# Optimization experiments

Hardware: AMD Instinct MI355X
Metric: run time of the kernel (lower is better)

Reference implementation:

```python
import jax, jax.numpy as jnp
import numpy as np

B, N, D, H = 32, 8192, 128, 128


def setup_inputs() -> dict:
    key = jax.random.key(0)
    ks = jax.random.split(key, 9)
    s = lambda k, shp, fan: jax.random.normal(k, shp, jnp.float32) / np.sqrt(fan)
    return {
        "x": jax.random.normal(ks[0], (B, N, D), jnp.float32),
        "Wg1": s(ks[1], (D, H), D), "bg1": jnp.zeros((H,), jnp.float32),
        "Wg2": s(ks[2], (H, 1), H), "bg2": jnp.zeros((1,), jnp.float32),
        "Wn1": s(ks[3], (D, H), D), "bn1": jnp.zeros((H,), jnp.float32),
        "Wn2": s(ks[4], (H, H), H), "bn2": jnp.zeros((H,), jnp.float32),
    }


def reference(x, Wg1, bg1, Wg2, bg2, Wn1, bn1, Wn2, bn2):
    # gate_nn: Linear -> SiLU -> Linear(->1); scores per node
    gate = jnp.einsum("bnd,dh->bnh", x, Wg1) + bg1
    gate = jax.nn.silu(gate)
    gate = jnp.einsum("bnh,ho->bno", gate, Wg2) + bg2  # [B,N,1]
    # nn: Linear -> SiLU -> Linear; transformed node features
    h = jax.nn.silu(jnp.einsum("bnd,dh->bnh", x, Wn1) + bn1)
    h = jnp.einsum("bnh,hk->bnk", h, Wn2) + bn2  # [B,N,H]
    # segment softmax over nodes of each graph (segments == batch dim here)
    attn = jax.nn.softmax(gate, axis=1)  # [B,N,1]
    # weighted-sum pooling per graph
    return jnp.sum(attn * h, axis=1)  # [B,H]
```

## Files before the change

kernel.cpp:

```cpp
#include <hip/hip_runtime.h>

#define B_ 32
#define N_ 8192
#define D_ 128
#define H_ 128
#define R_ (B_ * N_)

#define NBLK 4096

typedef _Float16 f16;
typedef __attribute__((ext_vector_type(4))) _Float16 f16x4;
typedef __attribute__((ext_vector_type(8))) _Float16 f16x8;
typedef __attribute__((ext_vector_type(4))) float f32x4;

static constexpr size_t WPACK_OFF = 0;
static constexpr size_t VPART_OFF = 65536;
static constexpr size_t SPART_OFF = VPART_OFF + (size_t)NBLK * 128 * 4;

__device__ __forceinline__ float silu_f(float v) {
    return v * __builtin_amdgcn_rcpf(1.0f + __expf(-v));
}

__device__ __forceinline__ f32x4 mfma16(f16x8 a, f16x8 b, f32x4 c) {
    return __builtin_amdgcn_mfma_f32_16x16x32_f16(a, b, c, 0, 0, 0);
}

__global__ void k0_prepack(const float* __restrict__ Wg1,
                           const float* __restrict__ Wn1,
                           f16* __restrict__ wp) {
    int tid = blockIdx.x * 256 + threadIdx.x;
    int m    = tid >> 14;
    int r    = tid & 16383;
    int j    = r & 7;
    int lane = (r >> 3) & 63;
    int kc   = (r >> 9) & 3;
    int nt   = r >> 11;
    int k = kc * 32 + (lane >> 4) * 8 + j;
    int n = nt * 16 + (lane & 15);
    const float* W = m ? Wn1 : Wg1;
    wp[tid] = (f16)W[k * 128 + n];
}

__global__ __launch_bounds__(256, 3) void k1_fused(
        const float* __restrict__ x,
        const float* __restrict__ bg1, const float* __restrict__ wg2,
        const float* __restrict__ bg2, const float* __restrict__ bn1,
        const f16* __restrict__ wp,
        float* __restrict__ vpart, float* __restrict__ spart) {
    __shared__ f16 xlds[64 * 128];
    __shared__ float gpart[4][64];

    const int tid  = threadIdx.x;
    const int w    = tid >> 6;
    const int lane = tid & 63;
    const int q    = lane >> 4;
    const int c    = lane & 15;

    const long rowbase = (long)blockIdx.x * 64;
    const float4* xg = (const float4*)x + rowbase * 32;
    float4 xv[8];
#pragma unroll
    for (int s = 0; s < 8; ++s) xv[s] = xg[s * 256 + tid];

    const f16x8* wpv = (const f16x8*)wp;
    f16x8 fg1[2][4], fn1[2][4];
#pragma unroll
    for (int s = 0; s < 2; ++s)
#pragma unroll
        for (int kc = 0; kc < 4; ++kc) {
            int base = ((2 * w + s) * 4 + kc) * 64 + lane;
            fg1[s][kc] = wpv[base];
            fn1[s][kc] = wpv[2048 + base];
        }
    float bg1q[2][4], wg2q[2][4], bn1q[2][4];
#pragma unroll
    for (int s = 0; s < 2; ++s)
#pragma unroll
        for (int r = 0; r < 4; ++r) {
            int col = (2 * w + s) * 16 + q * 4 + r;
            bg1q[s][r] = bg1[col];
            wg2q[s][r] = wg2[col];
            bn1q[s][r] = bn1[col];
        }
    const float bg2v = bg2[0];

    const int loh_e = (q * 16 + (c ^ q)) * 8;
    const int loh_o = (q * 16 + (c ^ (q | 4))) * 8;

#pragma unroll
    for (int s = 0; s < 8; ++s) {
        int e   = s * 256 + tid;
        int row = e >> 5, c4 = e & 31;
        int mt = row >> 4, cc = row & 15;
        int kc = c4 >> 3, qq = (c4 >> 1) & 3, j = (c4 & 1) * 4;
        int sw = (c4 >> 1) & 7;
        float4 vv = xv[s];
        f16x4 hv = {(f16)vv.x, (f16)vv.y, (f16)vv.z, (f16)vv.w};
        *(f16x4*)&xlds[((mt * 4 + kc) * 64 + qq * 16 + (cc ^ sw)) * 8 + j] = hv;
    }
    __syncthreads();

    f16x4 hq[4][2];
#pragma unroll
    for (int mt = 0; mt < 4; ++mt) {
        f16x8 a[4];
#pragma unroll
        for (int kc = 0; kc < 4; ++kc)
            a[kc] = *(const f16x8*)&xlds[(mt * 4 + kc) * 512 +
                                         ((kc & 1) ? loh_o : loh_e)];
        f32x4 ag[2] = {{0.f,0.f,0.f,0.f},{0.f,0.f,0.f,0.f}};
        f32x4 an[2] = {{0.f,0.f,0.f,0.f},{0.f,0.f,0.f,0.f}};
#pragma unroll
        for (int kc = 0; kc < 4; ++kc) {
#pragma unroll
            for (int s = 0; s < 2; ++s) {
                ag[s] = mfma16(fg1[s][kc], a[kc], ag[s]);
                an[s] = mfma16(fn1[s][kc], a[kc], an[s]);
            }
        }
#pragma unroll
        for (int s = 0; s < 2; ++s) {
            f16x4 h4;
#pragma unroll
            for (int r = 0; r < 4; ++r) h4[r] = (f16)silu_f(an[s][r] + bn1q[s][r]);
            hq[mt][s] = h4;
        }
        float p = 0.f;
#pragma unroll
        for (int s = 0; s < 2; ++s)
#pragma unroll
            for (int r = 0; r < 4; ++r)
                p += silu_f(ag[s][r] + bg1q[s][r]) * wg2q[s][r];
        p += __shfl_xor(p, 16);
        p += __shfl_xor(p, 32);
        if (lane < 16) gpart[w][mt * 16 + lane] = p;
    }
    __syncthreads();

    float e4[4];
#pragma unroll
    for (int mt = 0; mt < 4; ++mt) {
        float g = bg2v + gpart[0][mt * 16 + c] + gpart[1][mt * 16 + c]
                       + gpart[2][mt * 16 + c] + gpart[3][mt * 16 + c];
        e4[mt] = __expf(g);
    }

    float V[2][4] = {{0.f,0.f,0.f,0.f},{0.f,0.f,0.f,0.f}};
#pragma unroll
    for (int mt = 0; mt < 4; ++mt)
#pragma unroll
        for (int s = 0; s < 2; ++s)
#pragma unroll
            for (int r = 0; r < 4; ++r)
                V[s][r] += e4[mt] * (float)hq[mt][s][r];

#pragma unroll
    for (int m = 1; m < 16; m <<= 1)
#pragma unroll
        for (int s = 0; s < 2; ++s)
#pragma unroll
            for (int r = 0; r < 4; ++r) V[s][r] += __shfl_xor(V[s][r], m);
    if (c == 0) {
#pragma unroll
        for (int s = 0; s < 2; ++s) {
            float4 o = {V[s][0], V[s][1], V[s][2], V[s][3]};
            *(float4*)&vpart[(long)blockIdx.x * 128 + (2 * w + s) * 16 + q * 4] = o;
        }
    }
    if (w == 0) {
        float Sl = e4[0] + e4[1] + e4[2] + e4[3];
#pragma unroll
        for (int m = 1; m < 16; m <<= 1) Sl += __shfl_xor(Sl, m);
        if (lane == 0) spart[blockIdx.x] = Sl;
    }
}

__global__ void k2_combine(const float* __restrict__ vpart,
                           const float* __restrict__ spart,
                           const float* __restrict__ Wn2,
                           const float* __restrict__ bn2,
                           float* __restrict__ out) {
    const int b = blockIdx.x;
    const int t = threadIdx.x;

    __shared__ float pooled[128];
    __shared__ float sred2[2];

    float v = 0.f;
    if (t < 128) {
        const float* vp = vpart + (long)b * 128 * 128;
#pragma unroll 8
        for (int k = 0; k < 128; ++k) v += vp[k * 128 + t];
    }

    float s = (t < 128) ? spart[b * 128 + t] : 0.f;
#pragma unroll
    for (int m = 1; m < 64; m <<= 1) s += __shfl_xor(s, m);
    if (t < 128 && (t & 63) == 0) sred2[t >> 6] = s;
    __syncthreads();

    if (t < 128) pooled[t] = v / (sred2[0] + sred2[1]);
    __syncthreads();
    if (t < 128) {
        float acc = bn2[t];
#pragma unroll 8
        for (int k = 0; k < 128; ++k) acc += pooled[k] * Wn2[k * 128 + t];
        out[b * 128 + t] = acc;
    }
}

extern "C" void kernel_launch(void* const* d_in, const int* in_sizes, int n_in,
                              void* d_out, int out_size, void* d_ws, size_t ws_size,
                              hipStream_t stream) {
    const float* x   = (const float*)d_in[0];
    const float* Wg1 = (const float*)d_in[1];
    const float* bg1 = (const float*)d_in[2];
    const float* Wg2 = (const float*)d_in[3];
    const float* bg2 = (const float*)d_in[4];
    const float* Wn1 = (const float*)d_in[5];
    const float* bn1 = (const float*)d_in[6];
    const float* Wn2 = (const float*)d_in[7];
    const float* bn2 = (const float*)d_in[8];
    float* out = (float*)d_out;

    char* ws = (char*)d_ws;
    f16*   wp    = (f16*)(ws + WPACK_OFF);
    float* vpart = (float*)(ws + VPART_OFF);
    float* spart = (float*)(ws + SPART_OFF);

    k0_prepack<<<128, 256, 0, stream>>>(Wg1, Wn1, wp);
    k1_fused<<<NBLK, 256, 0, stream>>>(x, bg1, Wg2, bg2, bn1, wp, vpart, spart);
    k2_combine<<<32, 256, 0, stream>>>(vpart, spart, Wn2, bn2, out);
}
```

Measured before the change: 218.1 us.

## Use 512-thread blocks with one 16-column tile per wave in fused kernel

Doubles the block to 8 waves, each owning a single 16-column slice of the hidden dimension instead of two. The per-thread x loads, weight fragments, accumulators and stored activations are halved, which lowers register pressure and raises the resident-wave target (launch bounds 512,4). In exchange, each LDS x tile is read by twice as many waves, the gate partial sums are reduced across 8 slots instead of 4, and there is more per-block overhead.

Result: no change. 222.4 us (+1.9%).

```diff
diff --git a/kernel.cpp b/kernel.cpp
--- a/kernel.cpp
+++ b/kernel.cpp
@@ -41,14 +41,14 @@
     wp[tid] = (f16)W[k * 128 + n];
 }
 
-__global__ __launch_bounds__(256, 3) void k1_fused(
+__global__ __launch_bounds__(512, 4) void k1_fused(
         const float* __restrict__ x,
         const float* __restrict__ bg1, const float* __restrict__ wg2,
         const float* __restrict__ bg2, const float* __restrict__ bn1,
         const f16* __restrict__ wp,
         float* __restrict__ vpart, float* __restrict__ spart) {
     __shared__ f16 xlds[64 * 128];
-    __shared__ float gpart[4][64];
+    __shared__ float gpart[8][64];
 
     const int tid  = threadIdx.x;
     const int w    = tid >> 6;
@@ -58,38 +58,34 @@
 
     const long rowbase = (long)blockIdx.x * 64;
     const float4* xg = (const float4*)x + rowbase * 32;
-    float4 xv[8];
-#pragma unroll
-    for (int s = 0; s < 8; ++s) xv[s] = xg[s * 256 + tid];
+    float4 xv[4];
+#pragma unroll
+    for (int s = 0; s < 4; ++s) xv[s] = xg[s * 512 + tid];
 
     const f16x8* wpv = (const f16x8*)wp;
-    f16x8 fg1[2][4], fn1[2][4];
-#pragma unroll
-    for (int s = 0; s < 2; ++s)
-#pragma unroll
-        for (int kc = 0; kc < 4; ++kc) {
-            int base = ((2 * w + s) * 4 + kc) * 64 + lane;
-            fg1[s][kc] = wpv[base];
-            fn1[s][kc] = wpv[2048 + base];
-        }
-    float bg1q[2][4], wg2q[2][4], bn1q[2][4];
-#pragma unroll
-    for (int s = 0; s < 2; ++s)
-#pragma unroll
-        for (int r = 0; r < 4; ++r) {
-            int col = (2 * w + s) * 16 + q * 4 + r;
-            bg1q[s][r] = bg1[col];
-            wg2q[s][r] = wg2[col];
-            bn1q[s][r] = bn1[col];
-        }
+    f16x8 fg1[4], fn1[4];
+#pragma unroll
+    for (int kc = 0; kc < 4; ++kc) {
+        int base = (w * 4 + kc) * 64 + lane;
+        fg1[kc] = wpv[base];
+        fn1[kc] = wpv[2048 + base];
+    }
+    float bg1q[4], wg2q[4], bn1q[4];
+#pragma unroll
+    for (int r = 0; r < 4; ++r) {
+        int col = w * 16 + q * 4 + r;
+        bg1q[r] = bg1[col];
+        wg2q[r] = wg2[col];
+        bn1q[r] = bn1[col];
+    }
     const float bg2v = bg2[0];
 
     const int loh_e = (q * 16 + (c ^ q)) * 8;
     const int loh_o = (q * 16 + (c ^ (q | 4))) * 8;
 
 #pragma unroll
-    for (int s = 0; s < 8; ++s) {
-        int e   = s * 256 + tid;
+    for (int s = 0; s < 4; ++s) {
+        int e   = s * 512 + tid;
         int row = e >> 5, c4 = e & 31;
         int mt = row >> 4, cc = row & 15;
         int kc = c4 >> 3, qq = (c4 >> 1) & 3, j = (c4 & 1) * 4;
@@ -100,7 +96,7 @@
     }
     __syncthreads();
 
-    f16x4 hq[4][2];
+    f16x4 hq[4];
 #pragma unroll
     for (int mt = 0; mt < 4; ++mt) {
         f16x8 a[4];
@@ -108,29 +104,21 @@
         for (int kc = 0; kc < 4; ++kc)
             a[kc] = *(const f16x8*)&xlds[(mt * 4 + kc) * 512 +
                                          ((kc & 1) ? loh_o : loh_e)];
-        f32x4 ag[2] = {{0.f,0.f,0.f,0.f},{0.f,0.f,0.f,0.f}};
-        f32x4 an[2] = {{0.f,0.f,0.f,0.f},{0.f,0.f,0.f,0.f}};
+        f32x4 ag = {0.f, 0.f, 0.f, 0.f};
+        f32x4 an = {0.f, 0.f, 0.f, 0.f};
 #pragma unroll
         for (int kc = 0; kc < 4; ++kc) {
-#pragma unroll
-            for (int s = 0; s < 2; ++s) {
-                ag[s] = mfma16(fg1[s][kc], a[kc], ag[s]);
-                an[s] = mfma16(fn1[s][kc], a[kc], an[s]);
-            }
+            ag = mfma16(fg1[kc], a[kc], ag);
+            an = mfma16(fn1[kc], a[kc], an);
         }
-#pragma unroll
-        for (int s = 0; s < 2; ++s) {
-            f16x4 h4;
-#pragma unroll
-            for (int r = 0; r < 4; ++r) h4[r] = (f16)silu_f(an[s][r] + bn1q[s][r]);
-            hq[mt][s] = h4;
-        }
+        f16x4 h4;
+#pragma unroll
+        for (int r = 0; r < 4; ++r) h4[r] = (f16)silu_f(an[r] + bn1q[r]);
+        hq[mt] = h4;
         float p = 0.f;
 #pragma unroll
-        for (int s = 0; s < 2; ++s)
-#pragma unroll
-            for (int r = 0; r < 4; ++r)
-                p += silu_f(ag[s][r] + bg1q[s][r]) * wg2q[s][r];
+        for (int r = 0; r < 4; ++r)
+            p += silu_f(ag[r] + bg1q[r]) * wg2q[r];
         p += __shfl_xor(p, 16);
         p += __shfl_xor(p, 32);
         if (lane < 16) gpart[w][mt * 16 + lane] = p;
@@ -140,32 +128,26 @@
     float e4[4];
 #pragma unroll
     for (int mt = 0; mt < 4; ++mt) {
-        float g = bg2v + gpart[0][mt * 16 + c] + gpart[1][mt * 16 + c]
-                       + gpart[2][mt * 16 + c] + gpart[3][mt * 16 + c];
+        float g = bg2v;
+#pragma unroll
+        for (int k = 0; k < 8; ++k) g += gpart[k][mt * 16 + c];
         e4[mt] = __expf(g);
     }
 
-    float V[2][4] = {{0.f,0.f,0.f,0.f},{0.f,0.f,0.f,0.f}};
+    float V[4] = {0.f, 0.f, 0.f, 0.f};
 #pragma unroll
     for (int mt = 0; mt < 4; ++mt)
 #pragma unroll
-        for (int s = 0; s < 2; ++s)
-#pragma unroll
-            for (int r = 0; r < 4; ++r)
-                V[s][r] += e4[mt] * (float)hq[mt][s][r];
+        for (int r = 0; r < 4; ++r)
+            V[r] += e4[mt] * (float)hq[mt][r];
 
 #pragma unroll
     for (int m = 1; m < 16; m <<= 1)
 #pragma unroll
-        for (int s = 0; s < 2; ++s)
-#pragma unroll
-            for (int r = 0; r < 4; ++r) V[s][r] += __shfl_xor(V[s][r], m);
+        for (int r = 0; r < 4; ++r) V[r] += __shfl_xor(V[r], m);
     if (c == 0) {
-#pragma unroll
-        for (int s = 0; s < 2; ++s) {
-            float4 o = {V[s][0], V[s][1], V[s][2], V[s][3]};
-            *(float4*)&vpart[(long)blockIdx.x * 128 + (2 * w + s) * 16 + q * 4] = o;
-        }
+        float4 o = {V[0], V[1], V[2], V[3]};
+        *(float4*)&vpart[(long)blockIdx.x * 128 + w * 16 + q * 4] = o;
     }
     if (w == 0) {
         float Sl = e4[0] + e4[1] + e4[2] + e4[3];
@@ -229,6 +211,6 @@
     float* spart = (float*)(ws + SPART_OFF);
 
     k0_prepack<<<128, 256, 0, stream>>>(Wg1, Wn1, wp);
-    k1_fused<<<NBLK, 256, 0, stream>>>(x, bg1, Wg2, bg2, bn1, wp, vpart, spart);
+    k1_fused<<<NBLK, 512, 0, stream>>>(x, bg1, Wg2, bg2, bn1, wp, vpart, spart);
     k2_combine<<<32, 256, 0, stream>>>(vpart, spart, Wn2, bn2, out);
 }
```
